# Optimization experiments

Hardware: AMD Instinct MI355X
Metric: run time of the kernel (lower is better)

## Reference

```python
import jax, jax.numpy as jnp
import numpy as np

CONF_THRES = 0.4
IOU_THRES = 0.45
MAX_DET = 1000
MAX_WH = 7680.0  # class offset for non-agnostic NMS (yolov5 convention)
K = 2048         # pre-NMS candidate cap (>= MAX_DET)


def setup_inputs() -> dict:
    key = jax.random.key(0)
    k1, k2, k3, k4 = jax.random.split(key, 4)
    # uint8-valued image, stored as int32 (values 0..255)
    img = jax.random.randint(k1, (640, 640, 3), 0, 256, dtype=jnp.int32)
    B, N, NC = 8, 25200, 80
    xy = jax.random.uniform(k2, (B, N, 2)) * 640.0          # box centers in pixels
    wh = jax.random.uniform(k3, (B, N, 2)) * 80.0 + 4.0     # box sizes
    sc = jax.random.uniform(k4, (B, N, 1 + NC))             # objectness + class scores
    pred = jnp.concatenate([xy, wh, sc], axis=-1)           # [B, N, 85]
    return {"img": img, "pred": pred}


def _xywh2xyxy(x):
    xy, wh = x[..., :2], x[..., 2:4]
    return jnp.concatenate([xy - wh * 0.5, xy + wh * 0.5], axis=-1)


def _box_iou(a, b):
    # a: [K,4], b: [K,4] in xyxy
    lt = jnp.maximum(a[:, None, :2], b[None, :, :2])
    rb = jnp.minimum(a[:, None, 2:], b[None, :, 2:])
    wh = jnp.clip(rb - lt, 0.0)
    inter = wh[..., 0] * wh[..., 1]
    area_a = (a[:, 2] - a[:, 0]) * (a[:, 3] - a[:, 1])
    area_b = (b[:, 2] - b[:, 0]) * (b[:, 3] - b[:, 1])
    return inter / (area_a[:, None] + area_b[None, :] - inter + 1e-7)


def _nms_single(p):
    # p: [N, 5+nc]
    boxes = _xywh2xyxy(p[:, :4])                 # [N,4]
    conf_all = p[:, 5:] * p[:, 4:5]              # obj * cls
    conf = jnp.max(conf_all, axis=-1)            # best-class confidence [N]
    cls = jnp.argmax(conf_all, axis=-1).astype(p.dtype)
    scores = jnp.where(conf > CONF_THRES, conf, -1.0)
    # top-K candidates (score-sorted, padding gets score -1)
    top_s, idx = jax.lax.top_k(scores, K)
    b = boxes[idx]                               # [K,4] raw boxes
    c = cls[idx]                                 # [K] class ids (float)
    b_off = b + (c * MAX_WH)[:, None]            # class-offset boxes (agnostic_nms=False)
    iou = _box_iou(b_off, b_off)                 # [K,K]
    keep = top_s > CONF_THRES
    ar = jnp.arange(K)

    def body(i, keep):
        sup = keep[i] & (iou[i] > IOU_THRES) & (ar > i)
        return keep & jnp.logical_not(sup)

    keep = jax.lax.fori_loop(0, K, body, keep)
    fs = jnp.where(keep, top_s, -1.0)
    sel_s, sel = jax.lax.top_k(fs, MAX_DET)
    det = jnp.concatenate([b[sel], sel_s[:, None], c[sel][:, None]], axis=-1)  # [MAX_DET,6]
    return jnp.where((sel_s > CONF_THRES)[:, None], det, 0.0)


def reference(img, pred):
    # process_image: HWC -> CHW, BGR->RGB flip, float, /255, add batch dim
    x = img.astype(jnp.float32).transpose(2, 0, 1)[::-1] / 255.0
    x = x[None]                                  # [1,3,640,640]
    det = jax.vmap(_nms_single)(pred)[0]         # non_max_suppression(pred, ...)[0]
    return det, x
```

## Files before the change

kernel.cpp:

```cpp
#include <hip/hip_runtime.h>
#include <stdint.h>

#define N_ANCH 25200
#define NCLS   80
#define KSEL   2048
#define MAXDET 1000
#define CONF_T 0.4f
#define IOU_T  0.45f
#define MAX_WH 7680.0f
#define HBINS  512
#define HBASE  0xBE00u
#define NCAND_MAX 4096
#define NSB    788
#define NIB    400
#define SUPCAP 224

#define WS_SELSCORE  0
#define WS_SELBOX    8192
#define WS_DETCAND   40960
#define WS_CNT       92160
#define WS_KEYS      92480
#define WS_CLS       193280
#define WS_MASK      294912
#define WS_MTT       819200
#define WS_F         1343488
#define WS_CAND      294912

__global__ void __launch_bounds__(256)
prep_kernel(const float* __restrict__ pred0, uint32_t* __restrict__ keys,
            int* __restrict__ cls, uint32_t* __restrict__ cnt,
            uint32_t* __restrict__ fglob) {
    int tid = threadIdx.x;
    if (blockIdx.x == 0) {
        if (tid < 64) fglob[tid] = 0u;
        if (tid == 64) *cnt = 0u;
    }
    int lane = tid & 63, wave = tid >> 6;
    int g = lane >> 3, l = lane & 7;
    int a = blockIdx.x * 32 + wave * 8 + g;
    if (a >= N_ANCH) return;
    const float* p = pred0 + (size_t)a * 85;
    float obj = p[4];
    float v = -1e30f; int ci = 0;
    #pragma unroll
    for (int k = 0; k < 10; ++k) {
        int c = l + 8 * k;
        float x = p[5 + c] * obj;
        if (x > v) { v = x; ci = c; }
    }
    #pragma unroll
    for (int m = 1; m < 8; m <<= 1) {
        float ov = __shfl_xor(v, m, 64);
        int   oc = __shfl_xor(ci, m, 64);
        if (ov > v || (ov == v && oc < ci)) { v = ov; ci = oc; }
    }
    if (l == 0) {
        float score = (v > CONF_T) ? v : -1.0f;
        uint32_t bits = __float_as_uint(score);
        uint32_t key = (bits & 0x80000000u) ? ~bits : (bits | 0x80000000u);
        keys[a] = key; cls[a] = ci;
    }
}

__global__ void __launch_bounds__(256)
compact_kernel(const uint32_t* __restrict__ keys, uint32_t* __restrict__ cnt,
               unsigned long long* __restrict__ cand,
               const int* __restrict__ img, float* __restrict__ xout) {
    __shared__ uint32_t h[HBINS];
    __shared__ uint32_t s_lim;
    __shared__ int wtot[4];
    __shared__ int s_base;
    int tid = threadIdx.x;

    if (blockIdx.x >= 25) {
        int i = (blockIdx.x - 25) * 256 + tid;
        const int4* im4 = (const int4*)(img + (size_t)i * 12);
        int4 va = im4[0], vb = im4[1], vc = im4[2];
        int p0 = i * 4;
        float4 o0 = make_float4((float)va.z / 255.0f, (float)vb.y / 255.0f,
                                (float)vc.x / 255.0f, (float)vc.w / 255.0f);
        float4 o1 = make_float4((float)va.y / 255.0f, (float)vb.x / 255.0f,
                                (float)vb.w / 255.0f, (float)vc.z / 255.0f);
        float4 o2 = make_float4((float)va.x / 255.0f, (float)va.w / 255.0f,
                                (float)vb.z / 255.0f, (float)vc.y / 255.0f);
        *(float4*)(xout + p0)          = o0;
        *(float4*)(xout + 409600 + p0) = o1;
        *(float4*)(xout + 819200 + p0) = o2;
        return;
    }

    int lane = tid & 63, wv = tid >> 6;
    for (int b = tid; b < HBINS; b += 256) h[b] = 0u;
    if (tid == 0) s_lim = (HBASE << 16);
    __syncthreads();
    for (int i = tid; i < N_ANCH / 4; i += 256) {
        uint4 kk = ((const uint4*)keys)[i];
        if (kk.x >= (HBASE << 16)) atomicAdd(&h[(kk.x >> 16) - HBASE], 1u);
        if (kk.y >= (HBASE << 16)) atomicAdd(&h[(kk.y >> 16) - HBASE], 1u);
        if (kk.z >= (HBASE << 16)) atomicAdd(&h[(kk.z >> 16) - HBASE], 1u);
        if (kk.w >= (HBASE << 16)) atomicAdd(&h[(kk.w >> 16) - HBASE], 1u);
    }
    __syncthreads();
    for (int off = 1; off < HBINS; off <<= 1) {
        uint32_t a0 = h[tid] + ((tid + off < HBINS) ? h[tid + off] : 0u);
        uint32_t a1 = h[tid + 256] + ((tid + 256 + off < HBINS) ? h[tid + 256 + off] : 0u);
        __syncthreads();
        h[tid] = a0; h[tid + 256] = a1;
        __syncthreads();
    }
    for (int b = tid; b < HBINS; b += 256) {
        uint32_t sb  = h[b];
        uint32_t sb1 = (b < HBINS - 1) ? h[b + 1] : 0u;
        if (sb >= KSEL && sb1 < KSEL) s_lim = (uint32_t)(HBASE + b) << 16;
    }
    __syncthreads();
    uint32_t lim = s_lim;

    int i = blockIdx.x * 256 + tid;
    bool valid = (i < N_ANCH / 4);
    uint32_t ks[4] = {0, 0, 0, 0};
    int cm = 0;
    if (valid) {
        uint4 kk = ((const uint4*)keys)[i];
        ks[0] = kk.x; ks[1] = kk.y; ks[2] = kk.z; ks[3] = kk.w;
        #pragma unroll
        for (int j = 0; j < 4; ++j) cm += (ks[j] >= lim) ? 1 : 0;
    }
    int pre = cm;
    #pragma unroll
    for (int o = 1; o < 64; o <<= 1) {
        int v = __shfl_up(pre, o, 64);
        if (lane >= o) pre += v;
    }
    if (lane == 63) wtot[wv] = pre;
    __syncthreads();
    if (tid == 0) {
        int t = 0;
        #pragma unroll
        for (int w = 0; w < 4; ++w) { int x = wtot[w]; wtot[w] = t; t += x; }
        s_base = (t > 0) ? (int)atomicAdd(cnt, (uint32_t)t) : 0;
    }
    __syncthreads();
    int pos = s_base + wtot[wv] + (pre - cm);
    if (valid) {
        #pragma unroll
        for (int j = 0; j < 4; ++j) {
            if (ks[j] >= lim) {
                if (pos < NCAND_MAX)
                    cand[pos] = ((unsigned long long)ks[j] << 32)
                              | (uint32_t)(~(uint32_t)(i * 4 + j));
                ++pos;
            }
        }
    }
}

__global__ void __launch_bounds__(256)
rank_kernel(const uint32_t* __restrict__ cnt, const unsigned long long* __restrict__ cand,
            const float* __restrict__ pred0, const int* __restrict__ cls,
            float* __restrict__ sel_score, float4* __restrict__ selbox,
            float* __restrict__ det_cand) {
    __shared__ unsigned long long s_it[NCAND_MAX];
    __shared__ int s_n;
    int tid = threadIdx.x;
    if (tid == 0) s_n = (int)min(*cnt, (uint32_t)NCAND_MAX);
    __syncthreads();
    int n = s_n;
    int base = blockIdx.x * 32;
    if (base >= n) return;
    for (int i = tid; i < n; i += 256) s_it[i] = cand[i];
    __syncthreads();
    int grp = tid >> 4, s16 = tid & 15;
    #pragma unroll
    for (int o = 0; o < 2; ++o) {
        int it = base + grp + o * 16;
        if (it >= n) break;
        unsigned long long mine = s_it[it];
        int c = 0;
        for (int t = s16; t < n; t += 16)
            c += (s_it[t] > mine) ? 1 : 0;
        #pragma unroll
        for (int m = 1; m < 16; m <<= 1) c += __shfl_xor(c, m, 64);
        if (s16 == 0 && c < KSEL) {
            uint32_t key = (uint32_t)(mine >> 32);
            int ai = (int)(~(uint32_t)mine);
            uint32_t fb = (key & 0x80000000u) ? (key & 0x7FFFFFFFu) : ~key;
            float score = __uint_as_float(fb);
            const float* p = pred0 + (size_t)ai * 85;
            float x = p[0], y = p[1], w = p[2], hh = p[3];
            float x1 = x - w * 0.5f, y1 = y - hh * 0.5f;
            float x2 = x + w * 0.5f, y2 = y + hh * 0.5f;
            float cf = (float)cls[ai];
            float off = cf * MAX_WH;
            selbox[c] = make_float4(x1 + off, y1 + off, x2 + off, y2 + off);
            float* dc = det_cand + (size_t)c * 6;
            dc[0] = x1; dc[1] = y1; dc[2] = x2; dc[3] = y2; dc[4] = score; dc[5] = cf;
            sel_score[c] = score;
        }
    }
}

__global__ void __launch_bounds__(256)
mask_kernel(const float4* __restrict__ selbox, uint32_t* __restrict__ MT,
            uint32_t* __restrict__ MTT, uint32_t* __restrict__ fglob) {
    __shared__ float4 jb[32];
    int tid = threadIdx.x;
    int lane = tid & 63, wv = tid >> 6;
    int wi = blockIdx.x >> 3, rg = blockIdx.x & 7;

    if (tid < 32) jb[tid] = selbox[wi * 32 + tid];
    __syncthreads();
    int row = rg * 256 + tid;
    float4 a = selbox[row];
    float areaA = (a.z - a.x) * (a.w - a.y);
    uint32_t bits = 0;
    #pragma unroll 4
    for (int b = 0; b < 32; ++b) {
        int j = wi * 32 + b;
        if (j > row) {
            float4 q = jb[b];
            float lx = fmaxf(a.x, q.x), ly = fmaxf(a.y, q.y);
            float rx = fminf(a.z, q.z), ry = fminf(a.w, q.w);
            float ww = fmaxf(rx - lx, 0.0f), hh = fmaxf(ry - ly, 0.0f);
            float inter = ww * hh;
            float areaB = (q.z - q.x) * (q.w - q.y);
            float iou = inter / (areaA + areaB - inter + 1e-7f);
            if (iou > IOU_T) bits |= (1u << b);
        }
    }
    MT[(size_t)wi * 2048 + row] = bits;
    MTT[(size_t)row * 64 + wi] = bits;
    unsigned long long bm = __ballot(bits != 0u);
    if (lane == 0) {
        int wbase = rg * 8 + wv * 2;
        uint32_t lo = (uint32_t)bm, hi = (uint32_t)(bm >> 32);
        if (lo) atomicOr(&fglob[wbase], lo);
        if (hi) atomicOr(&fglob[wbase + 1], hi);
    }
}

__global__ void __launch_bounds__(256)
nms_kernel(const uint32_t* __restrict__ MT, const uint32_t* __restrict__ MTT,
           const uint32_t* __restrict__ fglob, const float* __restrict__ sel_score,
           const float* __restrict__ det_cand, float* __restrict__ det) {
    __shared__ uint32_t f[64];
    __shared__ int rowlist[SUPCAP];
    __shared__ uint32_t sup[SUPCAP * 64];
    __shared__ int s_R;
    int tid = threadIdx.x;

    if (tid < 64) {
        uint32_t fw = fglob[tid];
        f[tid] = fw;
        int cnt = __popc(fw);
        int pre = cnt;
        for (int o = 1; o < 64; o <<= 1) {
            int v = __shfl_up(pre, o, 64);
            if (tid >= o) pre += v;
        }
        int r = pre - cnt;
        while (fw) {
            int b = __ffs(fw) - 1; fw &= fw - 1;
            if (r < SUPCAP) rowlist[r] = tid * 32 + b;
            ++r;
        }
        if (tid == 63) s_R = pre;
    }
    __syncthreads();
    int R = s_R;
    bool sparse = (R <= SUPCAP);
    if (sparse) {
        for (int s = tid >> 6; s < R; s += 4)
            sup[s * 64 + (tid & 63)] = MTT[(size_t)rowlist[s] * 64 + (tid & 63)];
    }
    __syncthreads();
    if (tid >= 64) return;

    int lane = tid;
    uint32_t removed = 0;
    #pragma unroll
    for (int b = 0; b < 32; ++b)
        if (!(sel_score[lane * 32 + b] > CONF_T)) removed |= (1u << b);

    if (sparse) {
        int slot = 0;
        for (int w = 0; w < 64; ++w) {
            uint32_t fb = f[w];
            while (fb) {
                int b = __ffs(fb) - 1; fb &= fb - 1;
                uint32_t rv = __shfl((int)removed, w, 64);
                if (!((rv >> b) & 1u))
                    removed |= sup[slot * 64 + lane];
                ++slot;
            }
        }
    } else {
        for (int c = 0; c < 64; ++c) {
            const uint4* mb = (const uint4*)(MT + (size_t)lane * 2048 + c * 32);
            uint4 qa[8];
            #pragma unroll
            for (int k = 0; k < 8; ++k) qa[k] = mb[k];
            uint32_t rw[32];
            #pragma unroll
            for (int k = 0; k < 8; ++k) {
                rw[4*k] = qa[k].x; rw[4*k+1] = qa[k].y;
                rw[4*k+2] = qa[k].z; rw[4*k+3] = qa[k].w;
            }
            uint32_t keptmask = 0;
            if (lane == c) {
                uint32_t myrem = removed;
                #pragma unroll
                for (int b = 0; b < 32; ++b)
                    if (!((myrem >> b) & 1u)) { keptmask |= (1u << b); myrem |= rw[b]; }
            }
            keptmask = __shfl(keptmask, c, 64);
            #pragma unroll
            for (int b = 0; b < 32; ++b)
                if ((keptmask >> b) & 1u) removed |= rw[b];
        }
    }

    uint32_t kw = ~removed;
    int cnt2 = __popc(kw);
    int pre = cnt2;
    for (int o = 1; o < 64; o <<= 1) {
        int v = __shfl_up(pre, o, 64);
        if (lane >= o) pre += v;
    }
    int excl = pre - cnt2;
    int total = __shfl(pre, 63, 64);

    int r = excl;
    for (int b = 0; b < 32; ++b) {
        if ((kw >> b) & 1u) {
            if (r < MAXDET) {
                const float* src = det_cand + (size_t)(lane * 32 + b) * 6;
                float* dst = det + (size_t)r * 6;
                for (int j = 0; j < 6; ++j) dst[j] = src[j];
            }
            ++r;
        }
    }
    int start = total < MAXDET ? total : MAXDET;
    for (int z = start + lane; z < MAXDET; z += 64) {
        float* dst = det + (size_t)z * 6;
        for (int j = 0; j < 6; ++j) dst[j] = 0.0f;
    }
}

extern "C" void kernel_launch(void* const* d_in, const int* in_sizes, int n_in,
                              void* d_out, int out_size, void* d_ws, size_t ws_size,
                              hipStream_t stream) {
    const int*   img  = (const int*)d_in[0];
    const float* pred = (const float*)d_in[1];
    float* out = (float*)d_out;
    char* ws = (char*)d_ws;

    float*    sel_score = (float*)(ws + WS_SELSCORE);
    float4*   selbox    = (float4*)(ws + WS_SELBOX);
    float*    det_cand  = (float*)(ws + WS_DETCAND);
    uint32_t* cnt       = (uint32_t*)(ws + WS_CNT);
    uint32_t* keys      = (uint32_t*)(ws + WS_KEYS);
    int*      cls       = (int*)(ws + WS_CLS);
    uint32_t* MT        = (uint32_t*)(ws + WS_MASK);
    uint32_t* MTT       = (uint32_t*)(ws + WS_MTT);
    uint32_t* fglob     = (uint32_t*)(ws + WS_F);
    unsigned long long* cand = (unsigned long long*)(ws + WS_CAND);

    prep_kernel<<<NSB, 256, 0, stream>>>(pred, keys, cls, cnt, fglob);
    compact_kernel<<<25 + NIB, 256, 0, stream>>>(keys, cnt, cand,
                                                 img, out + MAXDET * 6);
    rank_kernel<<<128, 256, 0, stream>>>(cnt, cand, pred, cls,
                                         sel_score, selbox, det_cand);
    mask_kernel<<<512, 256, 0, stream>>>(selbox, MT, MTT, fglob);
    nms_kernel<<<1, 256, 0, stream>>>(MT, MTT, fglob, sel_score, det_cand, out);
}
```

Baseline: 148.0 us.

## Fuse five NMS pipeline kernels into one cooperative kernel with grid syncs

```diff
diff --git a/kernel.cpp b/kernel.cpp
--- a/kernel.cpp
+++ b/kernel.cpp
@@ -1,5 +1,8 @@
 #include <hip/hip_runtime.h>
+#include <hip/hip_cooperative_groups.h>
 #include <stdint.h>
+
+namespace cg = cooperative_groups;
 
 #define N_ANCH 25200
 #define NCLS   80
@@ -26,239 +29,239 @@
 #define WS_F         1343488
 #define WS_CAND      294912
 
-__global__ void __launch_bounds__(256)
-prep_kernel(const float* __restrict__ pred0, uint32_t* __restrict__ keys,
-            int* __restrict__ cls, uint32_t* __restrict__ cnt,
-            uint32_t* __restrict__ fglob) {
-    int tid = threadIdx.x;
-    if (blockIdx.x == 0) {
-        if (tid < 64) fglob[tid] = 0u;
-        if (tid == 64) *cnt = 0u;
-    }
-    int lane = tid & 63, wave = tid >> 6;
-    int g = lane >> 3, l = lane & 7;
-    int a = blockIdx.x * 32 + wave * 8 + g;
-    if (a >= N_ANCH) return;
-    const float* p = pred0 + (size_t)a * 85;
-    float obj = p[4];
-    float v = -1e30f; int ci = 0;
-    #pragma unroll
-    for (int k = 0; k < 10; ++k) {
-        int c = l + 8 * k;
-        float x = p[5 + c] * obj;
-        if (x > v) { v = x; ci = c; }
-    }
-    #pragma unroll
-    for (int m = 1; m < 8; m <<= 1) {
-        float ov = __shfl_xor(v, m, 64);
-        int   oc = __shfl_xor(ci, m, 64);
-        if (ov > v || (ov == v && oc < ci)) { v = ov; ci = oc; }
-    }
-    if (l == 0) {
-        float score = (v > CONF_T) ? v : -1.0f;
-        uint32_t bits = __float_as_uint(score);
-        uint32_t key = (bits & 0x80000000u) ? ~bits : (bits | 0x80000000u);
-        keys[a] = key; cls[a] = ci;
-    }
-}
-
-__global__ void __launch_bounds__(256)
-compact_kernel(const uint32_t* __restrict__ keys, uint32_t* __restrict__ cnt,
-               unsigned long long* __restrict__ cand,
-               const int* __restrict__ img, float* __restrict__ xout) {
-    __shared__ uint32_t h[HBINS];
+__global__ void __launch_bounds__(256, 2)
+fused_kernel(const float* __restrict__ pred0, const int* __restrict__ img,
+             float* __restrict__ xout,
+             uint32_t* __restrict__ keys, int* __restrict__ cls,
+             uint32_t* __restrict__ cnt, unsigned long long* __restrict__ cand,
+             float* __restrict__ sel_score, float4* __restrict__ selbox,
+             float* __restrict__ det_cand,
+             uint32_t* __restrict__ MT, uint32_t* __restrict__ MTT,
+             uint32_t* __restrict__ fglob, float* __restrict__ det) {
+    cg::grid_group grid = cg::this_grid();
+    __shared__ __align__(16) uint32_t smem[14336];
+    __shared__ float4 jb[32];
+    __shared__ uint32_t f_s[64];
+    __shared__ int rowlist[SUPCAP];
     __shared__ uint32_t s_lim;
     __shared__ int wtot[4];
     __shared__ int s_base;
-    int tid = threadIdx.x;
-
-    if (blockIdx.x >= 25) {
-        int i = (blockIdx.x - 25) * 256 + tid;
-        const int4* im4 = (const int4*)(img + (size_t)i * 12);
-        int4 va = im4[0], vb = im4[1], vc = im4[2];
-        int p0 = i * 4;
-        float4 o0 = make_float4((float)va.z / 255.0f, (float)vb.y / 255.0f,
-                                (float)vc.x / 255.0f, (float)vc.w / 255.0f);
-        float4 o1 = make_float4((float)va.y / 255.0f, (float)vb.x / 255.0f,
-                                (float)vb.w / 255.0f, (float)vc.z / 255.0f);
-        float4 o2 = make_float4((float)va.x / 255.0f, (float)va.w / 255.0f,
-                                (float)vb.z / 255.0f, (float)vc.y / 255.0f);
-        *(float4*)(xout + p0)          = o0;
-        *(float4*)(xout + 409600 + p0) = o1;
-        *(float4*)(xout + 819200 + p0) = o2;
-        return;
-    }
-
-    int lane = tid & 63, wv = tid >> 6;
-    for (int b = tid; b < HBINS; b += 256) h[b] = 0u;
-    if (tid == 0) s_lim = (HBASE << 16);
-    __syncthreads();
-    for (int i = tid; i < N_ANCH / 4; i += 256) {
-        uint4 kk = ((const uint4*)keys)[i];
-        if (kk.x >= (HBASE << 16)) atomicAdd(&h[(kk.x >> 16) - HBASE], 1u);
-        if (kk.y >= (HBASE << 16)) atomicAdd(&h[(kk.y >> 16) - HBASE], 1u);
-        if (kk.z >= (HBASE << 16)) atomicAdd(&h[(kk.z >> 16) - HBASE], 1u);
-        if (kk.w >= (HBASE << 16)) atomicAdd(&h[(kk.w >> 16) - HBASE], 1u);
-    }
-    __syncthreads();
-    for (int off = 1; off < HBINS; off <<= 1) {
-        uint32_t a0 = h[tid] + ((tid + off < HBINS) ? h[tid + off] : 0u);
-        uint32_t a1 = h[tid + 256] + ((tid + 256 + off < HBINS) ? h[tid + 256 + off] : 0u);
-        __syncthreads();
-        h[tid] = a0; h[tid + 256] = a1;
-        __syncthreads();
-    }
-    for (int b = tid; b < HBINS; b += 256) {
-        uint32_t sb  = h[b];
-        uint32_t sb1 = (b < HBINS - 1) ? h[b + 1] : 0u;
-        if (sb >= KSEL && sb1 < KSEL) s_lim = (uint32_t)(HBASE + b) << 16;
-    }
-    __syncthreads();
-    uint32_t lim = s_lim;
-
-    int i = blockIdx.x * 256 + tid;
-    bool valid = (i < N_ANCH / 4);
-    uint32_t ks[4] = {0, 0, 0, 0};
-    int cm = 0;
-    if (valid) {
-        uint4 kk = ((const uint4*)keys)[i];
-        ks[0] = kk.x; ks[1] = kk.y; ks[2] = kk.z; ks[3] = kk.w;
+    __shared__ int s_n;
+    __shared__ int s_R;
+
+    const int tid  = threadIdx.x;
+    const int bid  = blockIdx.x;
+    const int G    = gridDim.x;
+    const int lane = tid & 63, wv = tid >> 6;
+
+    if (bid == 0) {
+        if (tid < 64) fglob[tid] = 0u;
+        if (tid == 64) *cnt = 0u;
+    }
+
+    for (int vb = bid; vb < NSB + NIB; vb += G) {
+        if (vb < NSB) {
+            int g = lane >> 3, l = lane & 7;
+            int a = vb * 32 + wv * 8 + g;
+            if (a < N_ANCH) {
+                const float* p = pred0 + (size_t)a * 85;
+                float obj = p[4];
+                float v = -1e30f; int ci = 0;
+                #pragma unroll
+                for (int k = 0; k < 10; ++k) {
+                    int c = l + 8 * k;
+                    float x = p[5 + c] * obj;
+                    if (x > v) { v = x; ci = c; }
+                }
+                #pragma unroll
+                for (int m = 1; m < 8; m <<= 1) {
+                    float ov = __shfl_xor(v, m, 64);
+                    int   oc = __shfl_xor(ci, m, 64);
+                    if (ov > v || (ov == v && oc < ci)) { v = ov; ci = oc; }
+                }
+                if (l == 0) {
+                    float score = (v > CONF_T) ? v : -1.0f;
+                    uint32_t bits = __float_as_uint(score);
+                    uint32_t key = (bits & 0x80000000u) ? ~bits : (bits | 0x80000000u);
+                    keys[a] = key; cls[a] = ci;
+                }
+            }
+        } else {
+            int i = (vb - NSB) * 256 + tid;
+            const int4* im4 = (const int4*)(img + (size_t)i * 12);
+            int4 va = im4[0], vb4 = im4[1], vc = im4[2];
+            int p0 = i * 4;
+            float4 o0 = make_float4((float)va.z / 255.0f, (float)vb4.y / 255.0f,
+                                    (float)vc.x / 255.0f, (float)vc.w / 255.0f);
+            float4 o1 = make_float4((float)va.y / 255.0f, (float)vb4.x / 255.0f,
+                                    (float)vb4.w / 255.0f, (float)vc.z / 255.0f);
+            float4 o2 = make_float4((float)va.x / 255.0f, (float)va.w / 255.0f,
+                                    (float)vb4.z / 255.0f, (float)vc.y / 255.0f);
+            *(float4*)(xout + p0)          = o0;
+            *(float4*)(xout + 409600 + p0) = o1;
+            *(float4*)(xout + 819200 + p0) = o2;
+        }
+    }
+    grid.sync();
+
+    if (bid < 25) {
+        uint32_t* h = smem;
+        for (int b = tid; b < HBINS; b += 256) h[b] = 0u;
+        if (tid == 0) s_lim = (HBASE << 16);
+        __syncthreads();
+        for (int i = tid; i < N_ANCH / 4; i += 256) {
+            uint4 kk = ((const uint4*)keys)[i];
+            if (kk.x >= (HBASE << 16)) atomicAdd(&h[(kk.x >> 16) - HBASE], 1u);
+            if (kk.y >= (HBASE << 16)) atomicAdd(&h[(kk.y >> 16) - HBASE], 1u);
+            if (kk.z >= (HBASE << 16)) atomicAdd(&h[(kk.z >> 16) - HBASE], 1u);
+            if (kk.w >= (HBASE << 16)) atomicAdd(&h[(kk.w >> 16) - HBASE], 1u);
+        }
+        __syncthreads();
+        for (int off = 1; off < HBINS; off <<= 1) {
+            uint32_t a0 = h[tid] + ((tid + off < HBINS) ? h[tid + off] : 0u);
+            uint32_t a1 = h[tid + 256] + ((tid + 256 + off < HBINS) ? h[tid + 256 + off] : 0u);
+            __syncthreads();
+            h[tid] = a0; h[tid + 256] = a1;
+            __syncthreads();
+        }
+        for (int b = tid; b < HBINS; b += 256) {
+            uint32_t sb  = h[b];
+            uint32_t sb1 = (b < HBINS - 1) ? h[b + 1] : 0u;
+            if (sb >= KSEL && sb1 < KSEL) s_lim = (uint32_t)(HBASE + b) << 16;
+        }
+        __syncthreads();
+        uint32_t lim = s_lim;
+
+        int i = bid * 256 + tid;
+        bool valid = (i < N_ANCH / 4);
+        uint32_t ks[4] = {0, 0, 0, 0};
+        int cm = 0;
+        if (valid) {
+            uint4 kk = ((const uint4*)keys)[i];
+            ks[0] = kk.x; ks[1] = kk.y; ks[2] = kk.z; ks[3] = kk.w;
+            #pragma unroll
+            for (int j = 0; j < 4; ++j) cm += (ks[j] >= lim) ? 1 : 0;
+        }
+        int pre = cm;
         #pragma unroll
-        for (int j = 0; j < 4; ++j) cm += (ks[j] >= lim) ? 1 : 0;
-    }
-    int pre = cm;
-    #pragma unroll
-    for (int o = 1; o < 64; o <<= 1) {
-        int v = __shfl_up(pre, o, 64);
-        if (lane >= o) pre += v;
-    }
-    if (lane == 63) wtot[wv] = pre;
-    __syncthreads();
-    if (tid == 0) {
-        int t = 0;
-        #pragma unroll
-        for (int w = 0; w < 4; ++w) { int x = wtot[w]; wtot[w] = t; t += x; }
-        s_base = (t > 0) ? (int)atomicAdd(cnt, (uint32_t)t) : 0;
-    }
-    __syncthreads();
-    int pos = s_base + wtot[wv] + (pre - cm);
-    if (valid) {
-        #pragma unroll
-        for (int j = 0; j < 4; ++j) {
-            if (ks[j] >= lim) {
-                if (pos < NCAND_MAX)
-                    cand[pos] = ((unsigned long long)ks[j] << 32)
-                              | (uint32_t)(~(uint32_t)(i * 4 + j));
-                ++pos;
-            }
-        }
-    }
-}
-
-__global__ void __launch_bounds__(256)
-rank_kernel(const uint32_t* __restrict__ cnt, const unsigned long long* __restrict__ cand,
-            const float* __restrict__ pred0, const int* __restrict__ cls,
-            float* __restrict__ sel_score, float4* __restrict__ selbox,
-            float* __restrict__ det_cand) {
-    __shared__ unsigned long long s_it[NCAND_MAX];
-    __shared__ int s_n;
-    int tid = threadIdx.x;
-    if (tid == 0) s_n = (int)min(*cnt, (uint32_t)NCAND_MAX);
-    __syncthreads();
-    int n = s_n;
-    int base = blockIdx.x * 32;
-    if (base >= n) return;
-    for (int i = tid; i < n; i += 256) s_it[i] = cand[i];
-    __syncthreads();
-    int grp = tid >> 4, s16 = tid & 15;
-    #pragma unroll
-    for (int o = 0; o < 2; ++o) {
-        int it = base + grp + o * 16;
-        if (it >= n) break;
-        unsigned long long mine = s_it[it];
-        int c = 0;
-        for (int t = s16; t < n; t += 16)
-            c += (s_it[t] > mine) ? 1 : 0;
-        #pragma unroll
-        for (int m = 1; m < 16; m <<= 1) c += __shfl_xor(c, m, 64);
-        if (s16 == 0 && c < KSEL) {
-            uint32_t key = (uint32_t)(mine >> 32);
-            int ai = (int)(~(uint32_t)mine);
-            uint32_t fb = (key & 0x80000000u) ? (key & 0x7FFFFFFFu) : ~key;
-            float score = __uint_as_float(fb);
-            const float* p = pred0 + (size_t)ai * 85;
-            float x = p[0], y = p[1], w = p[2], hh = p[3];
-            float x1 = x - w * 0.5f, y1 = y - hh * 0.5f;
-            float x2 = x + w * 0.5f, y2 = y + hh * 0.5f;
-            float cf = (float)cls[ai];
-            float off = cf * MAX_WH;
-            selbox[c] = make_float4(x1 + off, y1 + off, x2 + off, y2 + off);
-            float* dc = det_cand + (size_t)c * 6;
-            dc[0] = x1; dc[1] = y1; dc[2] = x2; dc[3] = y2; dc[4] = score; dc[5] = cf;
-            sel_score[c] = score;
-        }
-    }
-}
-
-__global__ void __launch_bounds__(256)
-mask_kernel(const float4* __restrict__ selbox, uint32_t* __restrict__ MT,
-            uint32_t* __restrict__ MTT, uint32_t* __restrict__ fglob) {
-    __shared__ float4 jb[32];
-    int tid = threadIdx.x;
-    int lane = tid & 63, wv = tid >> 6;
-    int wi = blockIdx.x >> 3, rg = blockIdx.x & 7;
-
-    if (tid < 32) jb[tid] = selbox[wi * 32 + tid];
-    __syncthreads();
-    int row = rg * 256 + tid;
-    float4 a = selbox[row];
-    float areaA = (a.z - a.x) * (a.w - a.y);
-    uint32_t bits = 0;
-    #pragma unroll 4
-    for (int b = 0; b < 32; ++b) {
-        int j = wi * 32 + b;
-        if (j > row) {
-            float4 q = jb[b];
-            float lx = fmaxf(a.x, q.x), ly = fmaxf(a.y, q.y);
-            float rx = fminf(a.z, q.z), ry = fminf(a.w, q.w);
-            float ww = fmaxf(rx - lx, 0.0f), hh = fmaxf(ry - ly, 0.0f);
-            float inter = ww * hh;
-            float areaB = (q.z - q.x) * (q.w - q.y);
-            float iou = inter / (areaA + areaB - inter + 1e-7f);
-            if (iou > IOU_T) bits |= (1u << b);
-        }
-    }
-    MT[(size_t)wi * 2048 + row] = bits;
-    MTT[(size_t)row * 64 + wi] = bits;
-    unsigned long long bm = __ballot(bits != 0u);
-    if (lane == 0) {
-        int wbase = rg * 8 + wv * 2;
-        uint32_t lo = (uint32_t)bm, hi = (uint32_t)(bm >> 32);
-        if (lo) atomicOr(&fglob[wbase], lo);
-        if (hi) atomicOr(&fglob[wbase + 1], hi);
-    }
-}
-
-__global__ void __launch_bounds__(256)
-nms_kernel(const uint32_t* __restrict__ MT, const uint32_t* __restrict__ MTT,
-           const uint32_t* __restrict__ fglob, const float* __restrict__ sel_score,
-           const float* __restrict__ det_cand, float* __restrict__ det) {
-    __shared__ uint32_t f[64];
-    __shared__ int rowlist[SUPCAP];
-    __shared__ uint32_t sup[SUPCAP * 64];
-    __shared__ int s_R;
-    int tid = threadIdx.x;
+        for (int o = 1; o < 64; o <<= 1) {
+            int v = __shfl_up(pre, o, 64);
+            if (lane >= o) pre += v;
+        }
+        if (lane == 63) wtot[wv] = pre;
+        __syncthreads();
+        if (tid == 0) {
+            int t = 0;
+            #pragma unroll
+            for (int w = 0; w < 4; ++w) { int x = wtot[w]; wtot[w] = t; t += x; }
+            s_base = (t > 0) ? (int)atomicAdd(cnt, (uint32_t)t) : 0;
+        }
+        __syncthreads();
+        int pos = s_base + wtot[wv] + (pre - cm);
+        if (valid) {
+            #pragma unroll
+            for (int j = 0; j < 4; ++j) {
+                if (ks[j] >= lim) {
+                    if (pos < NCAND_MAX)
+                        cand[pos] = ((unsigned long long)ks[j] << 32)
+                                  | (uint32_t)(~(uint32_t)(i * 4 + j));
+                    ++pos;
+                }
+            }
+        }
+    }
+    grid.sync();
+
+    if (bid < 128) {
+        unsigned long long* s_it = reinterpret_cast<unsigned long long*>(smem);
+        if (tid == 0) s_n = (int)min(*cnt, (uint32_t)NCAND_MAX);
+        __syncthreads();
+        int n = s_n;
+        int base = bid * 32;
+        if (base < n) {
+            for (int i = tid; i < n; i += 256) s_it[i] = cand[i];
+            __syncthreads();
+            int grp = tid >> 4, s16 = tid & 15;
+            #pragma unroll
+            for (int o = 0; o < 2; ++o) {
+                int it = base + grp + o * 16;
+                if (it >= n) break;
+                unsigned long long mine = s_it[it];
+                int c = 0;
+                for (int t = s16; t < n; t += 16)
+                    c += (s_it[t] > mine) ? 1 : 0;
+                #pragma unroll
+                for (int m = 1; m < 16; m <<= 1) c += __shfl_xor(c, m, 64);
+                if (s16 == 0 && c < KSEL) {
+                    uint32_t key = (uint32_t)(mine >> 32);
+                    int ai = (int)(~(uint32_t)mine);
+                    uint32_t fb = (key & 0x80000000u) ? (key & 0x7FFFFFFFu) : ~key;
+                    float score = __uint_as_float(fb);
+                    const float* p = pred0 + (size_t)ai * 85;
+                    float x = p[0], y = p[1], w = p[2], hh = p[3];
+                    float x1 = x - w * 0.5f, y1 = y - hh * 0.5f;
+                    float x2 = x + w * 0.5f, y2 = y + hh * 0.5f;
+                    float cf = (float)cls[ai];
+                    float off = cf * MAX_WH;
+                    selbox[c] = make_float4(x1 + off, y1 + off, x2 + off, y2 + off);
+                    float* dc = det_cand + (size_t)c * 6;
+                    dc[0] = x1; dc[1] = y1; dc[2] = x2; dc[3] = y2;
+                    dc[4] = score; dc[5] = cf;
+                    sel_score[c] = score;
+                }
+            }
+        }
+    }
+    grid.sync();
+
+    for (int vb = bid; vb < 512; vb += G) {
+        int wi = vb >> 3, rg = vb & 7;
+        if (tid < 32) jb[tid] = selbox[wi * 32 + tid];
+        __syncthreads();
+        int row = rg * 256 + tid;
+        float4 a = selbox[row];
+        float areaA = (a.z - a.x) * (a.w - a.y);
+        uint32_t bits = 0;
+        #pragma unroll 4
+        for (int b = 0; b < 32; ++b) {
+            int j = wi * 32 + b;
+            if (j > row) {
+                float4 q = jb[b];
+                float lx = fmaxf(a.x, q.x), ly = fmaxf(a.y, q.y);
+                float rx = fminf(a.z, q.z), ry = fminf(a.w, q.w);
+                float ww = fmaxf(rx - lx, 0.0f), hh = fmaxf(ry - ly, 0.0f);
+                float inter = ww * hh;
+                float areaB = (q.z - q.x) * (q.w - q.y);
+                float iou = inter / (areaA + areaB - inter + 1e-7f);
+                if (iou > IOU_T) bits |= (1u << b);
+            }
+        }
+        MT[(size_t)wi * 2048 + row] = bits;
+        MTT[(size_t)row * 64 + wi] = bits;
+        unsigned long long bm = __ballot(bits != 0u);
+        if (lane == 0) {
+            int wbase = rg * 8 + wv * 2;
+            uint32_t lo = (uint32_t)bm, hi = (uint32_t)(bm >> 32);
+            if (lo) atomicOr(&fglob[wbase], lo);
+            if (hi) atomicOr(&fglob[wbase + 1], hi);
+        }
+        __syncthreads();
+    }
+    grid.sync();
+
+    if (bid != 0) return;
+    uint32_t* sup = smem;
 
     if (tid < 64) {
         uint32_t fw = fglob[tid];
-        f[tid] = fw;
-        int cnt = __popc(fw);
-        int pre = cnt;
+        f_s[tid] = fw;
+        int cnt1 = __popc(fw);
+        int pre = cnt1;
         for (int o = 1; o < 64; o <<= 1) {
             int v = __shfl_up(pre, o, 64);
             if (tid >= o) pre += v;
         }
-        int r = pre - cnt;
+        int r = pre - cnt1;
         while (fw) {
             int b = __ffs(fw) - 1; fw &= fw - 1;
             if (r < SUPCAP) rowlist[r] = tid * 32 + b;
@@ -276,7 +279,6 @@
     __syncthreads();
     if (tid >= 64) return;
 
-    int lane = tid;
     uint32_t removed = 0;
     #pragma unroll
     for (int b = 0; b < 32; ++b)
@@ -285,7 +287,7 @@
     if (sparse) {
         int slot = 0;
         for (int w = 0; w < 64; ++w) {
-            uint32_t fb = f[w];
+            uint32_t fb = f_s[w];
             while (fb) {
                 int b = __ffs(fb) - 1; fb &= fb - 1;
                 uint32_t rv = __shfl((int)removed, w, 64);
@@ -366,12 +368,22 @@
     uint32_t* MTT       = (uint32_t*)(ws + WS_MTT);
     uint32_t* fglob     = (uint32_t*)(ws + WS_F);
     unsigned long long* cand = (unsigned long long*)(ws + WS_CAND);
-
-    prep_kernel<<<NSB, 256, 0, stream>>>(pred, keys, cls, cnt, fglob);
-    compact_kernel<<<25 + NIB, 256, 0, stream>>>(keys, cnt, cand,
-                                                 img, out + MAXDET * 6);
-    rank_kernel<<<128, 256, 0, stream>>>(cnt, cand, pred, cls,
-                                         sel_score, selbox, det_cand);
-    mask_kernel<<<512, 256, 0, stream>>>(selbox, MT, MTT, fglob);
-    nms_kernel<<<1, 256, 0, stream>>>(MT, MTT, fglob, sel_score, det_cand, out);
+    float* xout = out + MAXDET * 6;
+
+    static int g_grid = 0;
+    if (g_grid == 0) {
+        int occ = 0;
+        if (hipOccupancyMaxActiveBlocksPerMultiprocessor(
+                &occ, fused_kernel, 256, 0) != hipSuccess || occ < 1)
+            occ = 1;
+        g_grid = occ * 256;
+        if (g_grid > 512) g_grid = 512;
+    }
+
+    void* args[] = {(void*)&pred, (void*)&img, (void*)&xout,
+                    (void*)&keys, (void*)&cls, (void*)&cnt, (void*)&cand,
+                    (void*)&sel_score, (void*)&selbox, (void*)&det_cand,
+                    (void*)&MT, (void*)&MTT, (void*)&fglob, (void*)&out};
+    hipLaunchCooperativeKernel(fused_kernel, dim3(g_grid), dim3(256),
+                               args, 0, stream);
 }
```

Result: slower. 359.3 us (+142.8%).

## Fuse NMS sweep into mask kernel via last-block-done atomic counter

Applied to the files above, without the earlier changes.

```diff
diff --git a/kernel.cpp b/kernel.cpp
--- a/kernel.cpp
+++ b/kernel.cpp
@@ -24,16 +24,20 @@
 #define WS_MASK      294912
 #define WS_MTT       819200
 #define WS_F         1343488
+#define WS_DONE      1343744
 #define WS_CAND      294912
+
+#define ST_U32(p, v) __hip_atomic_store((p), (v), __ATOMIC_RELAXED, __HIP_MEMORY_SCOPE_AGENT)
 
 __global__ void __launch_bounds__(256)
 prep_kernel(const float* __restrict__ pred0, uint32_t* __restrict__ keys,
             int* __restrict__ cls, uint32_t* __restrict__ cnt,
-            uint32_t* __restrict__ fglob) {
+            uint32_t* __restrict__ fglob, uint32_t* __restrict__ done) {
     int tid = threadIdx.x;
     if (blockIdx.x == 0) {
         if (tid < 64) fglob[tid] = 0u;
         if (tid == 64) *cnt = 0u;
+        if (tid == 65) *done = 0u;
     }
     int lane = tid & 63, wave = tid >> 6;
     int g = lane >> 3, l = lane & 7;
@@ -75,14 +79,14 @@
     if (blockIdx.x >= 25) {
         int i = (blockIdx.x - 25) * 256 + tid;
         const int4* im4 = (const int4*)(img + (size_t)i * 12);
-        int4 va = im4[0], vb = im4[1], vc = im4[2];
+        int4 va = im4[0], vb4 = im4[1], vc = im4[2];
         int p0 = i * 4;
-        float4 o0 = make_float4((float)va.z / 255.0f, (float)vb.y / 255.0f,
+        float4 o0 = make_float4((float)va.z / 255.0f, (float)vb4.y / 255.0f,
                                 (float)vc.x / 255.0f, (float)vc.w / 255.0f);
-        float4 o1 = make_float4((float)va.y / 255.0f, (float)vb.x / 255.0f,
-                                (float)vb.w / 255.0f, (float)vc.z / 255.0f);
+        float4 o1 = make_float4((float)va.y / 255.0f, (float)vb4.x / 255.0f,
+                                (float)vb4.w / 255.0f, (float)vc.z / 255.0f);
         float4 o2 = make_float4((float)va.x / 255.0f, (float)va.w / 255.0f,
-                                (float)vb.z / 255.0f, (float)vc.y / 255.0f);
+                                (float)vb4.z / 255.0f, (float)vc.y / 255.0f);
         *(float4*)(xout + p0)          = o0;
         *(float4*)(xout + 409600 + p0) = o1;
         *(float4*)(xout + 819200 + p0) = o2;
@@ -201,9 +205,16 @@
 }
 
 __global__ void __launch_bounds__(256)
-mask_kernel(const float4* __restrict__ selbox, uint32_t* __restrict__ MT,
-            uint32_t* __restrict__ MTT, uint32_t* __restrict__ fglob) {
+mask_nms_kernel(const float4* __restrict__ selbox, uint32_t* __restrict__ MT,
+                uint32_t* __restrict__ MTT, uint32_t* __restrict__ fglob,
+                uint32_t* __restrict__ done, const float* __restrict__ sel_score,
+                const float* __restrict__ det_cand, float* __restrict__ det) {
+    __shared__ __align__(16) uint32_t sup[SUPCAP * 64];
     __shared__ float4 jb[32];
+    __shared__ uint32_t f_s[64];
+    __shared__ int rowlist[SUPCAP];
+    __shared__ int s_R;
+    __shared__ int s_last;
     int tid = threadIdx.x;
     int lane = tid & 63, wv = tid >> 6;
     int wi = blockIdx.x >> 3, rg = blockIdx.x & 7;
@@ -228,8 +239,8 @@
             if (iou > IOU_T) bits |= (1u << b);
         }
     }
-    MT[(size_t)wi * 2048 + row] = bits;
-    MTT[(size_t)row * 64 + wi] = bits;
+    ST_U32(&MT[(size_t)wi * 2048 + row], bits);
+    ST_U32(&MTT[(size_t)row * 64 + wi], bits);
     unsigned long long bm = __ballot(bits != 0u);
     if (lane == 0) {
         int wbase = rg * 8 + wv * 2;
@@ -237,28 +248,27 @@
         if (lo) atomicOr(&fglob[wbase], lo);
         if (hi) atomicOr(&fglob[wbase + 1], hi);
     }
-}
-
-__global__ void __launch_bounds__(256)
-nms_kernel(const uint32_t* __restrict__ MT, const uint32_t* __restrict__ MTT,
-           const uint32_t* __restrict__ fglob, const float* __restrict__ sel_score,
-           const float* __restrict__ det_cand, float* __restrict__ det) {
-    __shared__ uint32_t f[64];
-    __shared__ int rowlist[SUPCAP];
-    __shared__ uint32_t sup[SUPCAP * 64];
-    __shared__ int s_R;
-    int tid = threadIdx.x;
+
+    __syncthreads();
+    if (tid == 0) {
+        uint32_t p = __hip_atomic_fetch_add(done, 1u, __ATOMIC_ACQ_REL,
+                                            __HIP_MEMORY_SCOPE_AGENT);
+        s_last = (p == 511u);
+    }
+    __syncthreads();
+    if (!s_last) return;
+    __threadfence();
 
     if (tid < 64) {
         uint32_t fw = fglob[tid];
-        f[tid] = fw;
-        int cnt = __popc(fw);
-        int pre = cnt;
+        f_s[tid] = fw;
+        int cnt1 = __popc(fw);
+        int pre = cnt1;
         for (int o = 1; o < 64; o <<= 1) {
             int v = __shfl_up(pre, o, 64);
             if (tid >= o) pre += v;
         }
-        int r = pre - cnt;
+        int r = pre - cnt1;
         while (fw) {
             int b = __ffs(fw) - 1; fw &= fw - 1;
             if (r < SUPCAP) rowlist[r] = tid * 32 + b;
@@ -270,13 +280,22 @@
     int R = s_R;
     bool sparse = (R <= SUPCAP);
     if (sparse) {
-        for (int s = tid >> 6; s < R; s += 4)
-            sup[s * 64 + (tid & 63)] = MTT[(size_t)rowlist[s] * 64 + (tid & 63)];
+        int s = tid >> 6, ln = tid & 63;
+        while (s + 12 < R) {
+            uint32_t a0 = MTT[(size_t)rowlist[s]      * 64 + ln];
+            uint32_t a1 = MTT[(size_t)rowlist[s + 4]  * 64 + ln];
+            uint32_t a2 = MTT[(size_t)rowlist[s + 8]  * 64 + ln];
+            uint32_t a3 = MTT[(size_t)rowlist[s + 12] * 64 + ln];
+            sup[s * 64 + ln] = a0;        sup[(s + 4) * 64 + ln] = a1;
+            sup[(s + 8) * 64 + ln] = a2;  sup[(s + 12) * 64 + ln] = a3;
+            s += 16;
+        }
+        for (; s < R; s += 4)
+            sup[s * 64 + ln] = MTT[(size_t)rowlist[s] * 64 + ln];
     }
     __syncthreads();
     if (tid >= 64) return;
 
-    int lane = tid;
     uint32_t removed = 0;
     #pragma unroll
     for (int b = 0; b < 32; ++b)
@@ -285,7 +304,7 @@
     if (sparse) {
         int slot = 0;
         for (int w = 0; w < 64; ++w) {
-            uint32_t fb = f[w];
+            uint32_t fb = f_s[w];
             while (fb) {
                 int b = __ffs(fb) - 1; fb &= fb - 1;
                 uint32_t rv = __shfl((int)removed, w, 64);
@@ -296,16 +315,10 @@
         }
     } else {
         for (int c = 0; c < 64; ++c) {
-            const uint4* mb = (const uint4*)(MT + (size_t)lane * 2048 + c * 32);
-            uint4 qa[8];
-            #pragma unroll
-            for (int k = 0; k < 8; ++k) qa[k] = mb[k];
             uint32_t rw[32];
-            #pragma unroll
-            for (int k = 0; k < 8; ++k) {
-                rw[4*k] = qa[k].x; rw[4*k+1] = qa[k].y;
-                rw[4*k+2] = qa[k].z; rw[4*k+3] = qa[k].w;
-            }
+            #pragma unroll 8
+            for (int b = 0; b < 32; ++b)
+                rw[b] = MT[(size_t)lane * 2048 + c * 32 + b];
             uint32_t keptmask = 0;
             if (lane == c) {
                 uint32_t myrem = removed;
@@ -365,13 +378,14 @@
     uint32_t* MT        = (uint32_t*)(ws + WS_MASK);
     uint32_t* MTT       = (uint32_t*)(ws + WS_MTT);
     uint32_t* fglob     = (uint32_t*)(ws + WS_F);
+    uint32_t* done      = (uint32_t*)(ws + WS_DONE);
     unsigned long long* cand = (unsigned long long*)(ws + WS_CAND);
-
-    prep_kernel<<<NSB, 256, 0, stream>>>(pred, keys, cls, cnt, fglob);
-    compact_kernel<<<25 + NIB, 256, 0, stream>>>(keys, cnt, cand,
-                                                 img, out + MAXDET * 6);
+    float* xout = out + MAXDET * 6;
+
+    prep_kernel<<<NSB, 256, 0, stream>>>(pred, keys, cls, cnt, fglob, done);
+    compact_kernel<<<25 + NIB, 256, 0, stream>>>(keys, cnt, cand, img, xout);
     rank_kernel<<<128, 256, 0, stream>>>(cnt, cand, pred, cls,
                                          sel_score, selbox, det_cand);
-    mask_kernel<<<512, 256, 0, stream>>>(selbox, MT, MTT, fglob);
-    nms_kernel<<<1, 256, 0, stream>>>(MT, MTT, fglob, sel_score, det_cand, out);
-}
+    mask_nms_kernel<<<512, 256, 0, stream>>>(selbox, MT, MTT, fglob, done,
+                                             sel_score, det_cand, out);
+}
```

Result: slower. 154.9 us (+4.7%).
